# Kernel tuning notes

Measured on AMD Instinct MI355X. Metric: run time of the kernel, lower is better.

## Reference

```python
import jax, jax.numpy as jnp
import numpy as np

B, S, HID, NH = 8, 1024, 1024, 16
HD = HID // NH  # 64
STR = 128
NEG = -1e10


def setup_inputs() -> dict:
    key = jax.random.key(0)
    ks = jax.random.split(key, 16)
    def lin(k, fan_in, fan_out):
        bound = 1.0 / np.sqrt(fan_in)
        kw, kb = jax.random.split(k)
        W = jax.random.uniform(kw, (fan_in, fan_out), jnp.float32, -bound, bound)
        b = jax.random.uniform(kb, (fan_out,), jnp.float32, -bound, bound)
        return W, b
    Wq, bq = lin(ks[0], HID, HID)
    Wk, bk = lin(ks[1], HID, HID)
    Wv, bv = lin(ks[2], HID, HID)
    Wsk, bsk = lin(ks[3], HID, STR)
    Wsv, bsv = lin(ks[4], HID, STR)
    Wo, bo = lin(ks[5], HID + STR, HID)
    return {
        "query": jax.random.normal(ks[6], (B, S, HID), jnp.float32),
        "key": jax.random.normal(ks[7], (B, S, HID), jnp.float32),
        "value": jax.random.normal(ks[8], (B, S, HID), jnp.float32),
        "x_rsa": jax.random.normal(ks[9], (B, S, STR), jnp.float32),
        "mask": jax.random.randint(ks[10], (B, 1, 1, S), 0, 2, jnp.int32),
        "rsa_mask": jax.random.randint(ks[11], (B, 1, 1, S), 0, 2, jnp.int32),
        "Wq": Wq, "bq": bq, "Wk": Wk, "bk": bk, "Wv": Wv, "bv": bv,
        "Wsk": Wsk, "bsk": bsk, "Wsv": Wsv, "bsv": bsv, "Wo": Wo, "bo": bo,
    }


def reference(query, key, value, x_rsa, mask, rsa_mask,
              Wq, bq, Wk, bk, Wv, bv, Wsk, bsk, Wsv, bsv, Wo, bo):
    scale = jnp.sqrt(jnp.float32(HD))
    Q = (query @ Wq + bq).reshape(B, S, NH, HD).transpose(0, 2, 1, 3)   # [B,NH,S,HD]
    K = (key @ Wk + bk).reshape(B, S, NH, HD).transpose(0, 2, 1, 3)
    V = (value @ Wv + bv).reshape(B, S, NH, HD).transpose(0, 2, 1, 3)
    str_K = (key @ Wsk + bsk)[:, None, :, :]    # [B,1,S,128]
    str_V = (value @ Wsv + bsv)[:, None, :, :]
    rsa_Q = x_rsa[:, None, :, :]                # [B,1,S,128]

    energy = jnp.einsum('bhqd,bhkd->bhqk', Q, K)           # [B,NH,S,S]
    rsa_energy = jnp.einsum('bhqd,bhkd->bhqk', rsa_Q, str_K)  # [B,1,S,S]
    # torch order: mask first, then divide by scale
    energy = jnp.where(mask == 0, NEG, energy) / scale
    rsa_energy = jnp.where(mask == 0, NEG, rsa_energy)
    rsa_energy = jnp.where(rsa_mask == 0, NEG, rsa_energy)  # str_scale == 1

    attention = jax.nn.softmax(energy, axis=-1)
    rsa_attention = jax.nn.softmax(rsa_energy, axis=-1)
    # dropout is identity in eval mode
    x = jnp.einsum('bhqk,bhkd->bhqd', attention, V)          # [B,NH,S,HD]
    rsa_x = jnp.einsum('bhqk,bhkd->bhqd', rsa_attention, str_V)  # [B,1,S,128]
    x = x.transpose(0, 2, 1, 3).reshape(B, S, HID)
    rsa_x = rsa_x.transpose(0, 2, 1, 3).reshape(B, S, STR)
    out = jnp.concatenate((x, rsa_x), axis=-1) @ Wo + bo     # [B,S,HID]
    return out, attention, rsa_attention
```

## Files before the change

### kernel.cpp

```cpp
#include <hip/hip_runtime.h>
#include <stdint.h>

typedef unsigned int u32;
typedef _Float16 f16_t;

typedef _Float16 f16x8 __attribute__((ext_vector_type(8)));
typedef float    f32x4 __attribute__((ext_vector_type(4)));

__device__ __forceinline__ f32x4 mfma16(f16x8 a, f16x8 b, f32x4 c){
  return __builtin_amdgcn_mfma_f32_16x16x32_f16(a, b, c, 0, 0, 0);
}
__device__ __forceinline__ float fexp2(float x){ return __builtin_amdgcn_exp2f(x); }

__device__ __forceinline__ void gl_lds16(const void* g, void* l){
  typedef const __attribute__((address_space(1))) void* gasp;
  typedef __attribute__((address_space(3))) void* lasp;
  gasp gp = reinterpret_cast<gasp>(reinterpret_cast<uintptr_t>(g));
  lasp lp = reinterpret_cast<lasp>(static_cast<u32>(reinterpret_cast<uintptr_t>(l)));
  __builtin_amdgcn_global_load_lds(gp, lp, 16, 0, 0);
}

template<int NBYTES, int ROWB, int NT>
__device__ __forceinline__ void stage_swz(const char* gbase, u32 gstrideB, char* lds, int tid){
  const u32 lane = (u32)(tid & 63);
  #pragma unroll
  for (int j = 0; j < NBYTES/(NT*16); ++j){
    u32 o   = (u32)(j*NT + tid) * 16u;
    u32 row = o / (u32)ROWB;
    u32 col = (o % (u32)ROWB) ^ ((row & 7u) << 4);
    gl_lds16(gbase + (size_t)row * gstrideB + col, lds + (o - lane*16u));
  }
}

__device__ __forceinline__ f16x8 frag_ld(const char* lds, u32 row, u32 rowB, u32 kbyte){
  return *reinterpret_cast<const f16x8*>(lds + (size_t)row*rowB + (kbyte ^ ((row & 7u) << 4)));
}

__device__ __forceinline__ void cvt8(const float* __restrict__ in, f16_t* __restrict__ out, u32 i){
  const f32x4* p = reinterpret_cast<const f32x4*>(in) + 2*(size_t)i;
  f32x4 a = p[0], b = p[1];
  f16x8 v;
  v[0]=(f16_t)a[0]; v[1]=(f16_t)a[1]; v[2]=(f16_t)a[2]; v[3]=(f16_t)a[3];
  v[4]=(f16_t)b[0]; v[5]=(f16_t)b[1]; v[6]=(f16_t)b[2]; v[7]=(f16_t)b[3];
  *(reinterpret_cast<f16x8*>(out) + i) = v;
}

__global__ void prep_all(const float* __restrict__ q, const float* __restrict__ k,
                         const float* __restrict__ v, const float* __restrict__ xr,
                         const int* __restrict__ mask, const int* __restrict__ rmask,
                         f16_t* __restrict__ qo, f16_t* __restrict__ ko,
                         f16_t* __restrict__ vo, f16_t* __restrict__ xo,
                         float* __restrict__ mb, float* __restrict__ rb){
  u32 b = blockIdx.x;
  if (b < 12288u){
    const float* in; f16_t* out; u32 base;
    if (b < 4096u){ in=q; out=qo; base=0u; }
    else if (b < 8192u){ in=k; out=ko; base=4096u; }
    else { in=v; out=vo; base=8192u; }
    cvt8(in, out, (b-base)*256u + threadIdx.x);
  } else if (b < 12800u){
    cvt8(xr, xo, (b-12288u)*256u + threadIdx.x);
  } else {
    u32 i = (b-12800u)*256u + threadIdx.x;
    int m = mask[i]; int r = rmask[i];
    mb[i] = m ? 0.0f : -1.0e9f;
    rb[i] = (m && r) ? 0.0f : -1.0e9f;
  }
}

__global__ void transpose_cvt(const float* __restrict__ W0, const float* __restrict__ W1,
                              const float* __restrict__ W2,
                              f16_t* __restrict__ T0, f16_t* __restrict__ T1, f16_t* __restrict__ T2,
                              u32 K, u32 N){
  const float* W = blockIdx.z==0 ? W0 : blockIdx.z==1 ? W1 : W2;
  f16_t* WT      = blockIdx.z==0 ? T0 : blockIdx.z==1 ? T1 : T2;
  __shared__ float tile[32][33];
  const u32 k0 = blockIdx.x*32u, n0 = blockIdx.y*32u;
  const int t = threadIdx.x;
  const int r = t >> 3, c4 = (t & 7) * 4;
  f32x4 v = *reinterpret_cast<const f32x4*>(W + (size_t)(k0 + r)*N + n0 + c4);
  tile[r][c4+0]=v[0]; tile[r][c4+1]=v[1]; tile[r][c4+2]=v[2]; tile[r][c4+3]=v[3];
  __syncthreads();
  union { f16_t x[4]; uint64_t u; } pk;
  #pragma unroll
  for (int j=0;j<4;++j) pk.x[j] = (f16_t)tile[c4+j][r];
  *reinterpret_cast<uint64_t*>(WT + (size_t)(n0 + r)*K + k0 + c4) = pk.u;
}

struct GArg { const void* A; const void* Bt; const float* bias; void* C; u32 ldc; int mode; };

__global__ __launch_bounds__(256, 2)
void gemm_bt(GArg g0, GArg g1, GArg g2, u32 lda, u32 ldb, u32 K)
{
  __shared__ char As[2][16384];
  __shared__ char Bs[2][16384];
  GArg g = blockIdx.z==0 ? g0 : blockIdx.z==1 ? g1 : g2;
  const int tid = threadIdx.x, lane = tid & 63, wid = tid >> 6;
  const int wr = wid >> 1, wc = wid & 1;
  const u32 bn = blockIdx.x * 128u, bm = blockIdx.y * 128u;
  const char* Ab = (const char*)((const f16_t*)g.A + (size_t)bm * lda);
  const char* Bb = (const char*)((const f16_t*)g.Bt + (size_t)bn * ldb);
  const u32 ldaB = lda*2u, ldbB = ldb*2u;

  f32x4 acc[4][4] = {};
  const int nt = (int)(K >> 6);

  stage_swz<16384,128,256>(Ab, ldaB, As[0], tid);
  stage_swz<16384,128,256>(Bb, ldbB, Bs[0], tid);
  __syncthreads();

  for (int t = 0; t < nt; ++t){
    if (t + 1 < nt){
      stage_swz<16384,128,256>(Ab + (size_t)(t+1)*128, ldaB, As[(t+1)&1], tid);
      stage_swz<16384,128,256>(Bb + (size_t)(t+1)*128, ldbB, Bs[(t+1)&1], tid);
    }
    const char* as = As[t&1]; const char* bs = Bs[t&1];
    f16x8 af[4][2], bf[4][2];
    #pragma unroll
    for (int mi=0; mi<4; ++mi)
      #pragma unroll
      for (int ks=0; ks<2; ++ks)
        af[mi][ks] = frag_ld(as, (u32)(wr*64 + mi*16 + (lane&15)), 128u, (u32)(ks*64 + ((lane>>4)<<4)));
    #pragma unroll
    for (int ni=0; ni<4; ++ni)
      #pragma unroll
      for (int ks=0; ks<2; ++ks)
        bf[ni][ks] = frag_ld(bs, (u32)(wc*64 + ni*16 + (lane&15)), 128u, (u32)(ks*64 + ((lane>>4)<<4)));
    #pragma unroll
    for (int mi=0; mi<4; ++mi)
      #pragma unroll
      for (int ni=0; ni<4; ++ni)
        #pragma unroll
        for (int ks=0; ks<2; ++ks)
          acc[mi][ni] = mfma16(af[mi][ks], bf[ni][ks], acc[mi][ni]);
    __syncthreads();
  }

  float bv[4];
  #pragma unroll
  for (int ni=0; ni<4; ++ni) bv[ni] = g.bias[bn + wc*64 + ni*16 + (lane&15)];

  #pragma unroll
  for (int mi=0; mi<4; ++mi){
    #pragma unroll
    for (int ni=0; ni<4; ++ni){
      u32 n  = bn + (u32)(wc*64 + ni*16 + (lane&15));
      u32 m0 = bm + (u32)(wr*64 + mi*16 + ((lane>>4)<<2));
      if (g.mode == 0){
        float* C = (float*)g.C;
        #pragma unroll
        for (int r=0;r<4;++r) C[(size_t)(m0+r)*g.ldc + n] = acc[mi][ni][r] + bv[ni];
      } else if (g.mode == 1){
        f16_t* C = (f16_t*)g.C;
        #pragma unroll
        for (int r=0;r<4;++r){
          u32 m = m0 + r;
          size_t idx = (((size_t)(m>>10)*16 + (n>>6))*1024 + (m&1023))*64 + (n&63);
          C[idx] = (f16_t)(acc[mi][ni][r] + bv[ni]);
        }
      } else if (g.mode == 2){
        f16_t* C = (f16_t*)g.C;
        size_t idx0 = ((size_t)(m0>>10)*g.ldc + n)*1024 + (m0 & 1023);
        union { f16_t v[4]; uint64_t u; } pk;
        #pragma unroll
        for (int r=0;r<4;++r) pk.v[r] = (f16_t)(acc[mi][ni][r] + bv[ni]);
        *reinterpret_cast<uint64_t*>(C + idx0) = pk.u;
      } else {
        f16_t* C = (f16_t*)g.C;
        #pragma unroll
        for (int r=0;r<4;++r) C[(size_t)(m0+r)*g.ldc + n] = (f16_t)(acc[mi][ni][r] + bv[ni]);
      }
    }
  }
}

template<int D, int BSHIFT, int SCALEBIT>
__global__ __launch_bounds__(512)
void attn_pass1(const f16_t* __restrict__ Qg, const f16_t* __restrict__ Kg,
                const float* __restrict__ mbias, float* __restrict__ statR)
{
  constexpr int S = 1024, KCH = 64;
  constexpr u32 ROWB = D*2;
  __shared__ char Qs[128*D*2];
  __shared__ char Ks[2][KCH*D*2];
  __shared__ float wsum[2][128];

  const int tid = threadIdx.x, lane = tid & 63, wid = tid >> 6;
  const int wr = wid >> 2, wc = wid & 3;
  const u32 qt = blockIdx.x, batch = blockIdx.y;
  const float scale = SCALEBIT ? 0.1803368801111244f : 1.4426950408889634f;
  const f16_t* qb = Qg + ((size_t)batch*S + (size_t)qt*128)*D;
  const f16_t* kb = Kg + (size_t)batch*S*D;
  const float* mbb = mbias + (size_t)(batch >> BSHIFT)*S;

  stage_swz<128*D*2, (int)ROWB, 512>((const char*)qb, ROWB, Qs, tid);
  stage_swz<KCH*D*2, (int)ROWB, 512>((const char*)kb, ROWB, Ks[0], tid);
  __syncthreads();

  float sacc[2] = {0.0f, 0.0f};
  constexpr int NCH = S / KCH;
  for (int ch = 0; ch < NCH; ++ch){
    if (ch + 1 < NCH)
      stage_swz<KCH*D*2, (int)ROWB, 512>((const char*)(kb + (size_t)(ch+1)*KCH*D), ROWB, Ks[(ch+1)&1], tid);
    const char* ks = Ks[ch&1];

    f32x4 mb[2];
    #pragma unroll
    for (int mi=0; mi<2; ++mi)
      mb[mi] = *reinterpret_cast<const f32x4*>(mbb + ch*KCH + wr*32 + mi*16 + ((lane>>4)<<2));

    f32x4 acc[2][2] = {};
    #pragma unroll
    for (int ksl=0; ksl<D/32; ++ksl){
      f16x8 af[2], bf[2];
      #pragma unroll
      for (int mi=0; mi<2; ++mi)
        af[mi] = frag_ld(ks, (u32)(wr*32 + mi*16 + (lane&15)), ROWB, (u32)(ksl*64 + ((lane>>4)<<4)));
      #pragma unroll
      for (int ni=0; ni<2; ++ni)
        bf[ni] = frag_ld(Qs, (u32)(wc*32 + ni*16 + (lane&15)), ROWB, (u32)(ksl*64 + ((lane>>4)<<4)));
      #pragma unroll
      for (int mi=0; mi<2; ++mi)
        #pragma unroll
        for (int ni=0; ni<2; ++ni)
          acc[mi][ni] = mfma16(af[mi], bf[ni], acc[mi][ni]);
    }

    #pragma unroll
    for (int ni=0; ni<2; ++ni)
      #pragma unroll
      for (int mi=0; mi<2; ++mi)
        #pragma unroll
        for (int r=0;r<4;++r)
          sacc[ni] += fexp2(acc[mi][ni][r]*scale + mb[mi][r]);

    __syncthreads();
  }

  #pragma unroll
  for (int ni=0; ni<2; ++ni){
    float s = sacc[ni];
    s += __shfl_xor(s, 16);
    s += __shfl_xor(s, 32);
    sacc[ni] = s;
  }
  if (lane < 16){
    wsum[wr][wc*32 + lane]      = sacc[0];
    wsum[wr][wc*32 + 16 + lane] = sacc[1];
  }
  __syncthreads();
  if (tid < 128)
    statR[(size_t)batch*S + (size_t)qt*128 + tid] = 1.0f / (wsum[0][tid] + wsum[1][tid]);
}

template<int D, int BSHIFT, int SCALEBIT>
__global__ __launch_bounds__(512)
void attn_pass2(const f16_t* __restrict__ Qg, const f16_t* __restrict__ Kg, const f16_t* __restrict__ Vtg,
                const float* __restrict__ mbias, const float* __restrict__ statR,
                float* __restrict__ attnOut,
                f16_t* __restrict__ xout, u32 xld, u32 xcolAdd)
{
  constexpr int S = 1024, KCH = 64;
  constexpr u32 ROWB = D*2;
  constexpr int MIPV = D/32;
  __shared__ char Qs[128*D*2];
  __shared__ char Ks[2][KCH*D*2];
  __shared__ char Vs[2][D*KCH*2];
  __shared__ float Pout[128*KCH];

  const int tid = threadIdx.x, lane = tid & 63, wid = tid >> 6;
  const int wr = wid >> 2, wc = wid & 3;
  const u32 qt = blockIdx.x, batch = blockIdx.y;
  const u32 bb = batch >> BSHIFT;
  const float scale = SCALEBIT ? 0.1803368801111244f : 1.4426950408889634f;
  const f16_t* qb = Qg + ((size_t)batch*S + (size_t)qt*128)*D;
  const f16_t* kb = Kg + (size_t)batch*S*D;
  const char* vtb = (const char*)(Vtg + (size_t)batch*D*S);
  const float* mbb = mbias + (size_t)bb*S;
  char* poutb = (char*)Pout;

  float rreg[2];
  #pragma unroll
  for (int ni=0; ni<2; ++ni){
    u32 q = qt*128u + (u32)(wc*32 + ni*16 + (lane&15));
    rreg[ni] = statR[(size_t)batch*S + q];
  }
  f32x4 accX[MIPV][2] = {};

  stage_swz<128*D*2, (int)ROWB, 512>((const char*)qb, ROWB, Qs, tid);
  stage_swz<KCH*D*2, (int)ROWB, 512>((const char*)kb, ROWB, Ks[0], tid);
  stage_swz<D*KCH*2, 128, 512>(vtb, (u32)(S*2), Vs[0], tid);
  __syncthreads();

  constexpr int NCH = S / KCH;
  for (int ch = 0; ch < NCH; ++ch){
    if (ch + 1 < NCH){
      stage_swz<KCH*D*2, (int)ROWB, 512>((const char*)(kb + (size_t)(ch+1)*KCH*D), ROWB, Ks[(ch+1)&1], tid);
      stage_swz<D*KCH*2, 128, 512>(vtb + (size_t)(ch+1)*KCH*2, (u32)(S*2), Vs[(ch+1)&1], tid);
    }
    const char* ks = Ks[ch&1];
    const char* vs = Vs[ch&1];

    f32x4 mb[2];
    #pragma unroll
    for (int mi=0; mi<2; ++mi)
      mb[mi] = *reinterpret_cast<const f32x4*>(mbb + ch*KCH + wr*32 + mi*16 + ((lane>>4)<<2));

    f32x4 acc[2][2] = {};
    #pragma unroll
    for (int ksl=0; ksl<D/32; ++ksl){
      f16x8 af[2], bf[2];
      #pragma unroll
      for (int mi=0; mi<2; ++mi)
        af[mi] = frag_ld(ks, (u32)(wr*32 + mi*16 + (lane&15)), ROWB, (u32)(ksl*64 + ((lane>>4)<<4)));
      #pragma unroll
      for (int ni=0; ni<2; ++ni)
        bf[ni] = frag_ld(Qs, (u32)(wc*32 + ni*16 + (lane&15)), ROWB, (u32)(ksl*64 + ((lane>>4)<<4)));
      #pragma unroll
      for (int mi=0; mi<2; ++mi)
        #pragma unroll
        for (int ni=0; ni<2; ++ni)
          acc[mi][ni] = mfma16(af[mi], bf[ni], acc[mi][ni]);
    }

    #pragma unroll
    for (int ni=0; ni<2; ++ni){
      u32 q = (u32)(wc*32 + ni*16 + (lane&15));
      #pragma unroll
      for (int mi=0; mi<2; ++mi){
        f32x4 pv;
        #pragma unroll
        for (int r=0;r<4;++r)
          pv[r] = fexp2(acc[mi][ni][r]*scale + mb[mi][r]) * rreg[ni];
        u32 k0b = (u32)(wr*32 + mi*16 + ((lane>>4)<<2)) * 4u;
        *reinterpret_cast<f32x4*>(poutb + (size_t)q*256 + (k0b ^ ((q&7u)<<4))) = pv;
      }
    }
    __syncthreads();

    #pragma unroll
    for (int ksl=0; ksl<2; ++ksl){
      f16x8 pb[2];
      #pragma unroll
      for (int ni=0; ni<2; ++ni){
        u32 q = (u32)(wc*32 + ni*16 + (lane&15));
        u32 kb0 = (u32)(ksl*128 + ((lane>>4)<<5));
        f32x4 p0 = *reinterpret_cast<const f32x4*>(poutb + (size_t)q*256 + ((kb0      ) ^ ((q&7u)<<4)));
        f32x4 p1 = *reinterpret_cast<const f32x4*>(poutb + (size_t)q*256 + ((kb0 + 16u) ^ ((q&7u)<<4)));
        f16x8 v;
        v[0]=(f16_t)p0[0]; v[1]=(f16_t)p0[1]; v[2]=(f16_t)p0[2]; v[3]=(f16_t)p0[3];
        v[4]=(f16_t)p1[0]; v[5]=(f16_t)p1[1]; v[6]=(f16_t)p1[2]; v[7]=(f16_t)p1[3];
        pb[ni] = v;
      }
      #pragma unroll
      for (int mi=0; mi<MIPV; ++mi){
        f16x8 vf = frag_ld(vs, (u32)(wr*(D/2) + mi*16 + (lane&15)), 128u, (u32)(ksl*64 + ((lane>>4)<<4)));
        #pragma unroll
        for (int ni=0; ni<2; ++ni)
          accX[mi][ni] = mfma16(vf, pb[ni], accX[mi][ni]);
      }
    }

    {
      u32 q2 = (u32)tid >> 2;
      float* abase = attnOut + (size_t)batch*S*S + ((size_t)qt*128 + q2)*S + (size_t)ch*KCH;
      #pragma unroll
      for (int j=0;j<4;++j){
        u32 kbyte = ((u32)(tid&3) + 4u*(u32)j)*16u;
        f32x4 v = *reinterpret_cast<const f32x4*>(poutb + (size_t)q2*256 + (kbyte ^ ((q2&7u)<<4)));
        *reinterpret_cast<f32x4*>(abase + (kbyte>>2)) = v;
      }
    }
    __syncthreads();
  }

  u32 col0 = (batch & ((1u<<BSHIFT)-1u)) * (u32)D + xcolAdd;
  #pragma unroll
  for (int mi=0; mi<MIPV; ++mi){
    #pragma unroll
    for (int ni=0; ni<2; ++ni){
      u32 d = (u32)(wr*(D/2) + mi*16 + ((lane>>4)<<2));
      u32 q = qt*128u + (u32)(wc*32 + ni*16 + (lane&15));
      union { f16_t v[4]; uint64_t u; } pk;
      #pragma unroll
      for (int r=0;r<4;++r) pk.v[r] = (f16_t)accX[mi][ni][r];
      *reinterpret_cast<uint64_t*>(xout + ((size_t)bb*S + q)*xld + col0 + d) = pk.u;
    }
  }
}

extern "C" void kernel_launch(void* const* d_in, const int* in_sizes, int n_in,
                              void* d_out, int out_size, void* d_ws, size_t ws_size,
                              hipStream_t stream)
{
  const float* query = (const float*)d_in[0];
  const float* key   = (const float*)d_in[1];
  const float* value = (const float*)d_in[2];
  const float* x_rsa = (const float*)d_in[3];
  const int*   mask  = (const int*)d_in[4];
  const int*   rmask = (const int*)d_in[5];
  const float* Wq = (const float*)d_in[6];  const float* bq = (const float*)d_in[7];
  const float* Wk = (const float*)d_in[8];  const float* bk = (const float*)d_in[9];
  const float* Wv = (const float*)d_in[10]; const float* bv = (const float*)d_in[11];
  const float* Wsk= (const float*)d_in[12]; const float* bsk= (const float*)d_in[13];
  const float* Wsv= (const float*)d_in[14]; const float* bsv= (const float*)d_in[15];
  const float* Wo = (const float*)d_in[16]; const float* bo = (const float*)d_in[17];

  char* ws = (char*)d_ws;
  size_t off = 0;
  auto alloc = [&](size_t bytes)->char*{ char* p = ws + off; off += (bytes + 255) & ~(size_t)255; return p; };

  f16_t* q16  = (f16_t*)alloc(16777216);
  f16_t* k16  = (f16_t*)alloc(16777216);
  f16_t* v16  = (f16_t*)alloc(16777216);
  f16_t* xrf  = (f16_t*)alloc(2097152);
  f16_t* wqT  = (f16_t*)alloc(2097152);
  f16_t* wkT  = (f16_t*)alloc(2097152);
  f16_t* wvT  = (f16_t*)alloc(2097152);
  f16_t* wskT = (f16_t*)alloc(262144);
  f16_t* wsvT = (f16_t*)alloc(262144);
  f16_t* woT  = (f16_t*)alloc(2359296);
  f16_t* Qh   = (f16_t*)alloc(16777216);
  f16_t* Kh   = (f16_t*)alloc(16777216);
  f16_t* Vth  = (f16_t*)alloc(16777216);
  f16_t* strK = (f16_t*)alloc(2097152);
  f16_t* strVt= (f16_t*)alloc(2097152);
  f16_t* conc = (f16_t*)alloc(18874368);
  float* stRm = (float*)alloc(524288);
  float* stRr = (float*)alloc(32768);
  float* mbias= (float*)alloc(32768);
  float* rbias= (float*)alloc(32768);

  prep_all<<<12832,256,0,stream>>>(query, key, value, x_rsa, mask, rmask,
                                   q16, k16, v16, xrf, mbias, rbias);
  transpose_cvt<<<dim3(32,32,3),256,0,stream>>>(Wq, Wk, Wv, wqT, wkT, wvT, 1024, 1024);
  transpose_cvt<<<dim3(32,4,2), 256,0,stream>>>(Wsk, Wsv, Wsv, wskT, wsvT, wsvT, 1024, 128);
  transpose_cvt<<<dim3(36,32,1),256,0,stream>>>(Wo, Wo, Wo, woT, woT, woT, 1152, 1024);

  {
    GArg gq{q16, wqT, bq, Qh,  0,    1};
    GArg gk{k16, wkT, bk, Kh,  0,    1};
    GArg gv{v16, wvT, bv, Vth, 1024, 2};
    gemm_bt<<<dim3(8,64,3),256,0,stream>>>(gq, gk, gv, 1024, 1024, 1024);
  }
  {
    GArg gk{k16, wskT, bsk, strK,  128, 3};
    GArg gv{v16, wsvT, bsv, strVt, 128, 2};
    gemm_bt<<<dim3(1,64,2),256,0,stream>>>(gk, gv, gv, 1024, 1024, 1024);
  }

  attn_pass1<64,4,1> <<<dim3(8,128),512,0,stream>>>(Qh,  Kh,   mbias, stRm);
  attn_pass1<128,0,0><<<dim3(8,8),  512,0,stream>>>(xrf, strK, rbias, stRr);

  float* outp  = (float*)d_out;
  float* attnp = outp + 8388608;
  float* rsap  = outp + 8388608 + 134217728;

  attn_pass2<64,4,1> <<<dim3(8,128),512,0,stream>>>(Qh,  Kh,   Vth,   mbias, stRm, attnp, conc, 1152, 0);
  attn_pass2<128,0,0><<<dim3(8,8),  512,0,stream>>>(xrf, strK, strVt, rbias, stRr, rsap,  conc, 1152, 1024);

  {
    GArg go{conc, woT, bo, outp, 1024, 0};
    gemm_bt<<<dim3(8,64,1),256,0,stream>>>(go, go, go, 1152, 1152, 1152);
  }

  (void)in_sizes; (void)n_in; (void)out_size; (void)ws_size;
}
```

Measured before the change: 428.7 us.

## Merge launches: fuse weight transposes, GEMMs and attention passes into fewer kernels

Weight transpose-conversion moves into the prep kernel. All five projection GEMMs run in one grid. The main and RSA attention passes each become a single launch, which cuts kernel count and the tail idle time between small launches. The RSA path now uses a 32-key chunk so both attention variants fit in a shared LDS size. The GEMM swaps MFMA operands for the non-transposed outputs so the epilogue can write vectorized rows, and the swizzle is generalized to the row width. This adds branchy dispatch and larger static LDS for the attention kernels, which may lower occupancy for the main heads.

```diff
diff --git a/kernel.cpp b/kernel.cpp
--- a/kernel.cpp
+++ b/kernel.cpp
@@ -27,13 +27,19 @@
   for (int j = 0; j < NBYTES/(NT*16); ++j){
     u32 o   = (u32)(j*NT + tid) * 16u;
     u32 row = o / (u32)ROWB;
-    u32 col = (o % (u32)ROWB) ^ ((row & 7u) << 4);
+    u32 col = (o % (u32)ROWB) ^ ((row & ((u32)(ROWB>>4)-1u)) << 4);
     gl_lds16(gbase + (size_t)row * gstrideB + col, lds + (o - lane*16u));
   }
 }
 
-__device__ __forceinline__ f16x8 frag_ld(const char* lds, u32 row, u32 rowB, u32 kbyte){
-  return *reinterpret_cast<const f16x8*>(lds + (size_t)row*rowB + (kbyte ^ ((row & 7u) << 4)));
+template<int ROWB>
+__device__ __forceinline__ u32 swzb(u32 row, u32 col){
+  return col ^ ((row & ((u32)(ROWB>>4)-1u)) << 4);
+}
+
+template<int ROWB>
+__device__ __forceinline__ f16x8 frag_ld(const char* lds, u32 row, u32 kbyte){
+  return *reinterpret_cast<const f16x8*>(lds + (size_t)row*ROWB + swzb<ROWB>(row, kbyte));
 }
 
 __device__ __forceinline__ void cvt8(const float* __restrict__ in, f16_t* __restrict__ out, u32 i){
@@ -50,7 +56,14 @@
                          const int* __restrict__ mask, const int* __restrict__ rmask,
                          f16_t* __restrict__ qo, f16_t* __restrict__ ko,
                          f16_t* __restrict__ vo, f16_t* __restrict__ xo,
-                         float* __restrict__ mb, float* __restrict__ rb){
+                         float* __restrict__ mb, float* __restrict__ rb,
+                         const float* __restrict__ Wq, const float* __restrict__ Wk,
+                         const float* __restrict__ Wv, const float* __restrict__ Wsk,
+                         const float* __restrict__ Wsv, const float* __restrict__ Wo,
+                         f16_t* __restrict__ wqT, f16_t* __restrict__ wkT, f16_t* __restrict__ wvT,
+                         f16_t* __restrict__ wskT, f16_t* __restrict__ wsvT, f16_t* __restrict__ woT)
+{
+  __shared__ float tile[32][33];
   u32 b = blockIdx.x;
   if (b < 12288u){
     const float* in; f16_t* out; u32 base;
@@ -60,50 +73,65 @@
     cvt8(in, out, (b-base)*256u + threadIdx.x);
   } else if (b < 12800u){
     cvt8(xr, xo, (b-12288u)*256u + threadIdx.x);
-  } else {
+  } else if (b < 12832u){
     u32 i = (b-12800u)*256u + threadIdx.x;
     int m = mask[i]; int r = rmask[i];
     mb[i] = m ? 0.0f : -1.0e9f;
     rb[i] = (m && r) ? 0.0f : -1.0e9f;
-  }
-}
-
-__global__ void transpose_cvt(const float* __restrict__ W0, const float* __restrict__ W1,
-                              const float* __restrict__ W2,
-                              f16_t* __restrict__ T0, f16_t* __restrict__ T1, f16_t* __restrict__ T2,
-                              u32 K, u32 N){
-  const float* W = blockIdx.z==0 ? W0 : blockIdx.z==1 ? W1 : W2;
-  f16_t* WT      = blockIdx.z==0 ? T0 : blockIdx.z==1 ? T1 : T2;
-  __shared__ float tile[32][33];
-  const u32 k0 = blockIdx.x*32u, n0 = blockIdx.y*32u;
-  const int t = threadIdx.x;
-  const int r = t >> 3, c4 = (t & 7) * 4;
-  f32x4 v = *reinterpret_cast<const f32x4*>(W + (size_t)(k0 + r)*N + n0 + c4);
-  tile[r][c4+0]=v[0]; tile[r][c4+1]=v[1]; tile[r][c4+2]=v[2]; tile[r][c4+3]=v[3];
-  __syncthreads();
-  union { f16_t x[4]; uint64_t u; } pk;
-  #pragma unroll
-  for (int j=0;j<4;++j) pk.x[j] = (f16_t)tile[c4+j][r];
-  *reinterpret_cast<uint64_t*>(WT + (size_t)(n0 + r)*K + k0 + c4) = pk.u;
-}
-
-struct GArg { const void* A; const void* Bt; const float* bias; void* C; u32 ldc; int mode; };
+  } else {
+    u32 t = b - 12832u;
+    const float* W; f16_t* WT; u32 K, N, i, j;
+    if (t < 3072u){
+      u32 w = t >> 10, l = t & 1023u;
+      W = w==0 ? Wq : w==1 ? Wk : Wv;
+      WT = w==0 ? wqT : w==1 ? wkT : wvT;
+      K = 1024u; N = 1024u; i = l & 31u; j = l >> 5;
+    } else if (t < 3328u){
+      u32 l = t - 3072u;
+      W  = l < 128u ? Wsk : Wsv;
+      WT = l < 128u ? wskT : wsvT;
+      l &= 127u;
+      K = 1024u; N = 128u; i = l & 31u; j = l >> 5;
+    } else {
+      u32 l = t - 3328u;
+      W = Wo; WT = woT; K = 1152u; N = 1024u; i = l % 36u; j = l / 36u;
+    }
+    const u32 k0 = i*32u, n0 = j*32u;
+    const int tt = threadIdx.x;
+    const int r = tt >> 3, c4 = (tt & 7) * 4;
+    f32x4 val = *reinterpret_cast<const f32x4*>(W + (size_t)(k0 + r)*N + n0 + c4);
+    tile[r][c4+0]=val[0]; tile[r][c4+1]=val[1]; tile[r][c4+2]=val[2]; tile[r][c4+3]=val[3];
+    __syncthreads();
+    union { f16_t x[4]; uint64_t u; } pk;
+    #pragma unroll
+    for (int jj=0;jj<4;++jj) pk.x[jj] = (f16_t)tile[c4+jj][r];
+    *reinterpret_cast<uint64_t*>(WT + (size_t)(n0 + r)*K + k0 + c4) = pk.u;
+  }
+}
+
+struct GArg { const f16_t* A; const f16_t* Bt; const float* bias; void* C; u32 lda, ldb, ldc, K; int mode; };
+struct GPack { GArg g[5]; int single; };
 
 __global__ __launch_bounds__(256, 2)
-void gemm_bt(GArg g0, GArg g1, GArg g2, u32 lda, u32 ldb, u32 K)
+void gemm_bt(GPack p)
 {
   __shared__ char As[2][16384];
   __shared__ char Bs[2][16384];
-  GArg g = blockIdx.z==0 ? g0 : blockIdx.z==1 ? g1 : g2;
+  GArg g; u32 bn;
+  const u32 bm = blockIdx.y * 128u;
+  if (p.single >= 0){ g = p.g[p.single]; bn = blockIdx.x*128u; }
+  else if (blockIdx.z == 0u){ if (blockIdx.x >= 2u) return; g = p.g[3u+blockIdx.x]; bn = 0u; }
+  else { g = p.g[blockIdx.z-1u]; bn = blockIdx.x*128u; }
+
   const int tid = threadIdx.x, lane = tid & 63, wid = tid >> 6;
   const int wr = wid >> 1, wc = wid & 1;
-  const u32 bn = blockIdx.x * 128u, bm = blockIdx.y * 128u;
-  const char* Ab = (const char*)((const f16_t*)g.A + (size_t)bm * lda);
-  const char* Bb = (const char*)((const f16_t*)g.Bt + (size_t)bn * ldb);
-  const u32 ldaB = lda*2u, ldbB = ldb*2u;
+  const char* Ab = (const char*)(g.A + (size_t)bm * g.lda);
+  const char* Bb = (const char*)(g.Bt + (size_t)bn * g.ldb);
+  const u32 ldaB = g.lda*2u, ldbB = g.ldb*2u;
+  const bool swp = (g.mode != 2);
 
   f32x4 acc[4][4] = {};
-  const int nt = (int)(K >> 6);
+  const int nt = (int)(g.K >> 6);
 
   stage_swz<16384,128,256>(Ab, ldaB, As[0], tid);
   stage_swz<16384,128,256>(Bb, ldbB, Bs[0], tid);
@@ -120,107 +148,133 @@
     for (int mi=0; mi<4; ++mi)
       #pragma unroll
       for (int ks=0; ks<2; ++ks)
-        af[mi][ks] = frag_ld(as, (u32)(wr*64 + mi*16 + (lane&15)), 128u, (u32)(ks*64 + ((lane>>4)<<4)));
+        af[mi][ks] = frag_ld<128>(as, (u32)(wr*64 + mi*16 + (lane&15)), (u32)(ks*64 + ((lane>>4)<<4)));
     #pragma unroll
     for (int ni=0; ni<4; ++ni)
       #pragma unroll
       for (int ks=0; ks<2; ++ks)
-        bf[ni][ks] = frag_ld(bs, (u32)(wc*64 + ni*16 + (lane&15)), 128u, (u32)(ks*64 + ((lane>>4)<<4)));
-    #pragma unroll
-    for (int mi=0; mi<4; ++mi)
-      #pragma unroll
-      for (int ni=0; ni<4; ++ni)
-        #pragma unroll
-        for (int ks=0; ks<2; ++ks)
-          acc[mi][ni] = mfma16(af[mi][ks], bf[ni][ks], acc[mi][ni]);
+        bf[ni][ks] = frag_ld<128>(bs, (u32)(wc*64 + ni*16 + (lane&15)), (u32)(ks*64 + ((lane>>4)<<4)));
+    if (swp){
+      #pragma unroll
+      for (int mi=0; mi<4; ++mi)
+        #pragma unroll
+        for (int ni=0; ni<4; ++ni)
+          #pragma unroll
+          for (int ks=0; ks<2; ++ks)
+            acc[mi][ni] = mfma16(bf[ni][ks], af[mi][ks], acc[mi][ni]);
+    } else {
+      #pragma unroll
+      for (int mi=0; mi<4; ++mi)
+        #pragma unroll
+        for (int ni=0; ni<4; ++ni)
+          #pragma unroll
+          for (int ks=0; ks<2; ++ks)
+            acc[mi][ni] = mfma16(af[mi][ks], bf[ni][ks], acc[mi][ni]);
+    }
     __syncthreads();
   }
 
-  float bv[4];
-  #pragma unroll
-  for (int ni=0; ni<4; ++ni) bv[ni] = g.bias[bn + wc*64 + ni*16 + (lane&15)];
-
-  #pragma unroll
-  for (int mi=0; mi<4; ++mi){
-    #pragma unroll
-    for (int ni=0; ni<4; ++ni){
-      u32 n  = bn + (u32)(wc*64 + ni*16 + (lane&15));
-      u32 m0 = bm + (u32)(wr*64 + mi*16 + ((lane>>4)<<2));
-      if (g.mode == 0){
-        float* C = (float*)g.C;
-        #pragma unroll
-        for (int r=0;r<4;++r) C[(size_t)(m0+r)*g.ldc + n] = acc[mi][ni][r] + bv[ni];
-      } else if (g.mode == 1){
-        f16_t* C = (f16_t*)g.C;
-        #pragma unroll
-        for (int r=0;r<4;++r){
-          u32 m = m0 + r;
-          size_t idx = (((size_t)(m>>10)*16 + (n>>6))*1024 + (m&1023))*64 + (n&63);
-          C[idx] = (f16_t)(acc[mi][ni][r] + bv[ni]);
-        }
-      } else if (g.mode == 2){
-        f16_t* C = (f16_t*)g.C;
+  if (g.mode == 2){
+    float bv[4];
+    #pragma unroll
+    for (int ni=0; ni<4; ++ni) bv[ni] = g.bias[bn + wc*64 + ni*16 + (lane&15)];
+    f16_t* C = (f16_t*)g.C;
+    #pragma unroll
+    for (int mi=0; mi<4; ++mi){
+      #pragma unroll
+      for (int ni=0; ni<4; ++ni){
+        u32 n  = bn + (u32)(wc*64 + ni*16 + (lane&15));
+        u32 m0 = bm + (u32)(wr*64 + mi*16 + ((lane>>4)<<2));
         size_t idx0 = ((size_t)(m0>>10)*g.ldc + n)*1024 + (m0 & 1023);
         union { f16_t v[4]; uint64_t u; } pk;
         #pragma unroll
         for (int r=0;r<4;++r) pk.v[r] = (f16_t)(acc[mi][ni][r] + bv[ni]);
         *reinterpret_cast<uint64_t*>(C + idx0) = pk.u;
-      } else {
-        f16_t* C = (f16_t*)g.C;
-        #pragma unroll
-        for (int r=0;r<4;++r) C[(size_t)(m0+r)*g.ldc + n] = (f16_t)(acc[mi][ni][r] + bv[ni]);
       }
     }
-  }
-}
-
-template<int D, int BSHIFT, int SCALEBIT>
-__global__ __launch_bounds__(512)
-void attn_pass1(const f16_t* __restrict__ Qg, const f16_t* __restrict__ Kg,
-                const float* __restrict__ mbias, float* __restrict__ statR)
-{
-  constexpr int S = 1024, KCH = 64;
-  constexpr u32 ROWB = D*2;
-  __shared__ char Qs[128*D*2];
-  __shared__ char Ks[2][KCH*D*2];
-  __shared__ float wsum[2][128];
-
-  const int tid = threadIdx.x, lane = tid & 63, wid = tid >> 6;
+  } else {
+    f32x4 bf4[4];
+    #pragma unroll
+    for (int ni=0; ni<4; ++ni)
+      bf4[ni] = *reinterpret_cast<const f32x4*>(g.bias + bn + wc*64 + ni*16 + ((lane>>4)<<2));
+    #pragma unroll
+    for (int mi=0; mi<4; ++mi){
+      u32 m = bm + (u32)(wr*64 + mi*16 + (lane&15));
+      #pragma unroll
+      for (int ni=0; ni<4; ++ni){
+        u32 n0 = bn + (u32)(wc*64 + ni*16 + ((lane>>4)<<2));
+        if (g.mode == 0){
+          float* C = (float*)g.C;
+          f32x4 v = acc[mi][ni] + bf4[ni];
+          *reinterpret_cast<f32x4*>(C + (size_t)m*g.ldc + n0) = v;
+        } else if (g.mode == 1){
+          f16_t* C = (f16_t*)g.C;
+          size_t idx = (((size_t)(m>>10)*16 + (n0>>6))*1024 + (m&1023))*64 + (n0&63);
+          union { f16_t v[4]; uint64_t u; } pk;
+          #pragma unroll
+          for (int r=0;r<4;++r) pk.v[r] = (f16_t)(acc[mi][ni][r] + bf4[ni][r]);
+          *reinterpret_cast<uint64_t*>(C + idx) = pk.u;
+        } else {
+          f16_t* C = (f16_t*)g.C;
+          union { f16_t v[4]; uint64_t u; } pk;
+          #pragma unroll
+          for (int r=0;r<4;++r) pk.v[r] = (f16_t)(acc[mi][ni][r] + bf4[ni][r]);
+          *reinterpret_cast<uint64_t*>(C + (size_t)m*g.ldc + n0) = pk.u;
+        }
+      }
+    }
+  }
+}
+
+template<int D, int KCH, int BSHIFT, int SCALEBIT>
+__device__ __forceinline__ void pass1_body(char* smem,
+    const f16_t* __restrict__ Qg, const f16_t* __restrict__ Kg,
+    const float* __restrict__ mbias, float* __restrict__ statR,
+    const int tid, const u32 qt, const u32 batch)
+{
+  constexpr int S = 1024;
+  constexpr int ROWB = D*2;
+  constexpr int MI = KCH/32;
+  char* Qs  = smem;
+  char* Ks0 = smem + 128*ROWB;
+  char* Ks1 = Ks0 + KCH*ROWB;
+  float* wsum = (float*)(Ks1 + KCH*ROWB);
+
+  const int lane = tid & 63, wid = tid >> 6;
   const int wr = wid >> 2, wc = wid & 3;
-  const u32 qt = blockIdx.x, batch = blockIdx.y;
   const float scale = SCALEBIT ? 0.1803368801111244f : 1.4426950408889634f;
   const f16_t* qb = Qg + ((size_t)batch*S + (size_t)qt*128)*D;
   const f16_t* kb = Kg + (size_t)batch*S*D;
   const float* mbb = mbias + (size_t)(batch >> BSHIFT)*S;
 
-  stage_swz<128*D*2, (int)ROWB, 512>((const char*)qb, ROWB, Qs, tid);
-  stage_swz<KCH*D*2, (int)ROWB, 512>((const char*)kb, ROWB, Ks[0], tid);
+  stage_swz<128*ROWB, ROWB, 512>((const char*)qb, ROWB, Qs, tid);
+  stage_swz<KCH*ROWB, ROWB, 512>((const char*)kb, ROWB, Ks0, tid);
   __syncthreads();
 
   float sacc[2] = {0.0f, 0.0f};
   constexpr int NCH = S / KCH;
   for (int ch = 0; ch < NCH; ++ch){
     if (ch + 1 < NCH)
-      stage_swz<KCH*D*2, (int)ROWB, 512>((const char*)(kb + (size_t)(ch+1)*KCH*D), ROWB, Ks[(ch+1)&1], tid);
-    const char* ks = Ks[ch&1];
-
-    f32x4 mb[2];
-    #pragma unroll
-    for (int mi=0; mi<2; ++mi)
-      mb[mi] = *reinterpret_cast<const f32x4*>(mbb + ch*KCH + wr*32 + mi*16 + ((lane>>4)<<2));
-
-    f32x4 acc[2][2] = {};
+      stage_swz<KCH*ROWB, ROWB, 512>((const char*)(kb + (size_t)(ch+1)*KCH*D), ROWB, ((ch+1)&1)?Ks1:Ks0, tid);
+    const char* ks = (ch&1) ? Ks1 : Ks0;
+
+    f32x4 mb[MI];
+    #pragma unroll
+    for (int mi=0; mi<MI; ++mi)
+      mb[mi] = *reinterpret_cast<const f32x4*>(mbb + ch*KCH + wr*(KCH/2) + mi*16 + ((lane>>4)<<2));
+
+    f32x4 acc[MI][2] = {};
     #pragma unroll
     for (int ksl=0; ksl<D/32; ++ksl){
-      f16x8 af[2], bf[2];
-      #pragma unroll
-      for (int mi=0; mi<2; ++mi)
-        af[mi] = frag_ld(ks, (u32)(wr*32 + mi*16 + (lane&15)), ROWB, (u32)(ksl*64 + ((lane>>4)<<4)));
+      f16x8 af[MI], bf[2];
+      #pragma unroll
+      for (int mi=0; mi<MI; ++mi)
+        af[mi] = frag_ld<ROWB>(ks, (u32)(wr*(KCH/2) + mi*16 + (lane&15)), (u32)(ksl*64 + ((lane>>4)<<4)));
       #pragma unroll
       for (int ni=0; ni<2; ++ni)
-        bf[ni] = frag_ld(Qs, (u32)(wc*32 + ni*16 + (lane&15)), ROWB, (u32)(ksl*64 + ((lane>>4)<<4)));
-      #pragma unroll
-      for (int mi=0; mi<2; ++mi)
+        bf[ni] = frag_ld<ROWB>(Qs, (u32)(wc*32 + ni*16 + (lane&15)), (u32)(ksl*64 + ((lane>>4)<<4)));
+      #pragma unroll
+      for (int mi=0; mi<MI; ++mi)
         #pragma unroll
         for (int ni=0; ni<2; ++ni)
           acc[mi][ni] = mfma16(af[mi], bf[ni], acc[mi][ni]);
@@ -229,7 +283,7 @@
     #pragma unroll
     for (int ni=0; ni<2; ++ni)
       #pragma unroll
-      for (int mi=0; mi<2; ++mi)
+      for (int mi=0; mi<MI; ++mi)
         #pragma unroll
         for (int r=0;r<4;++r)
           sacc[ni] += fexp2(acc[mi][ni][r]*scale + mb[mi][r]);
@@ -245,39 +299,42 @@
     sacc[ni] = s;
   }
   if (lane < 16){
-    wsum[wr][wc*32 + lane]      = sacc[0];
-    wsum[wr][wc*32 + 16 + lane] = sacc[1];
+    wsum[wr*128 + wc*32 + lane]      = sacc[0];
+    wsum[wr*128 + wc*32 + 16 + lane] = sacc[1];
   }
   __syncthreads();
   if (tid < 128)
-    statR[(size_t)batch*S + (size_t)qt*128 + tid] = 1.0f / (wsum[0][tid] + wsum[1][tid]);
-}
-
-template<int D, int BSHIFT, int SCALEBIT>
-__global__ __launch_bounds__(512)
-void attn_pass2(const f16_t* __restrict__ Qg, const f16_t* __restrict__ Kg, const f16_t* __restrict__ Vtg,
-                const float* __restrict__ mbias, const float* __restrict__ statR,
-                float* __restrict__ attnOut,
-                f16_t* __restrict__ xout, u32 xld, u32 xcolAdd)
-{
-  constexpr int S = 1024, KCH = 64;
-  constexpr u32 ROWB = D*2;
+    statR[(size_t)batch*S + (size_t)qt*128 + tid] = 1.0f / (wsum[tid] + wsum[128 + tid]);
+}
+
+template<int D, int KCH, int BSHIFT, int SCALEBIT>
+__device__ __forceinline__ void pass2_body(char* smem,
+    const f16_t* __restrict__ Qg, const f16_t* __restrict__ Kg, const f16_t* __restrict__ Vtg,
+    const float* __restrict__ mbias, const float* __restrict__ statR,
+    float* __restrict__ attnOut, f16_t* __restrict__ xout, u32 xld, u32 xcolAdd,
+    const int tid, const u32 qt, const u32 batch)
+{
+  constexpr int S = 1024;
+  constexpr int ROWB = D*2;
+  constexpr int ROWBV = KCH*2;
+  constexpr int PROW = KCH*4;
+  constexpr int MI = KCH/32;
   constexpr int MIPV = D/32;
-  __shared__ char Qs[128*D*2];
-  __shared__ char Ks[2][KCH*D*2];
-  __shared__ char Vs[2][D*KCH*2];
-  __shared__ float Pout[128*KCH];
-
-  const int tid = threadIdx.x, lane = tid & 63, wid = tid >> 6;
+  char* Qs  = smem;
+  char* Ks0 = Qs + 128*ROWB;
+  char* Ks1 = Ks0 + KCH*ROWB;
+  char* Vs0 = Ks1 + KCH*ROWB;
+  char* Vs1 = Vs0 + D*KCH*2;
+  char* poutb = Vs1 + D*KCH*2;
+
+  const int lane = tid & 63, wid = tid >> 6;
   const int wr = wid >> 2, wc = wid & 3;
-  const u32 qt = blockIdx.x, batch = blockIdx.y;
   const u32 bb = batch >> BSHIFT;
   const float scale = SCALEBIT ? 0.1803368801111244f : 1.4426950408889634f;
   const f16_t* qb = Qg + ((size_t)batch*S + (size_t)qt*128)*D;
   const f16_t* kb = Kg + (size_t)batch*S*D;
   const char* vtb = (const char*)(Vtg + (size_t)batch*D*S);
   const float* mbb = mbias + (size_t)bb*S;
-  char* poutb = (char*)Pout;
 
   float rreg[2];
   #pragma unroll
@@ -287,37 +344,37 @@
   }
   f32x4 accX[MIPV][2] = {};
 
-  stage_swz<128*D*2, (int)ROWB, 512>((const char*)qb, ROWB, Qs, tid);
-  stage_swz<KCH*D*2, (int)ROWB, 512>((const char*)kb, ROWB, Ks[0], tid);
-  stage_swz<D*KCH*2, 128, 512>(vtb, (u32)(S*2), Vs[0], tid);
+  stage_swz<128*ROWB, ROWB, 512>((const char*)qb, ROWB, Qs, tid);
+  stage_swz<KCH*ROWB, ROWB, 512>((const char*)kb, ROWB, Ks0, tid);
+  stage_swz<D*KCH*2, ROWBV, 512>(vtb, (u32)(S*2), Vs0, tid);
   __syncthreads();
 
   constexpr int NCH = S / KCH;
   for (int ch = 0; ch < NCH; ++ch){
     if (ch + 1 < NCH){
-      stage_swz<KCH*D*2, (int)ROWB, 512>((const char*)(kb + (size_t)(ch+1)*KCH*D), ROWB, Ks[(ch+1)&1], tid);
-      stage_swz<D*KCH*2, 128, 512>(vtb + (size_t)(ch+1)*KCH*2, (u32)(S*2), Vs[(ch+1)&1], tid);
-    }
-    const char* ks = Ks[ch&1];
-    const char* vs = Vs[ch&1];
-
-    f32x4 mb[2];
-    #pragma unroll
-    for (int mi=0; mi<2; ++mi)
-      mb[mi] = *reinterpret_cast<const f32x4*>(mbb + ch*KCH + wr*32 + mi*16 + ((lane>>4)<<2));
-
-    f32x4 acc[2][2] = {};
+      stage_swz<KCH*ROWB, ROWB, 512>((const char*)(kb + (size_t)(ch+1)*KCH*D), ROWB, ((ch+1)&1)?Ks1:Ks0, tid);
+      stage_swz<D*KCH*2, ROWBV, 512>(vtb + (size_t)(ch+1)*KCH*2, (u32)(S*2), ((ch+1)&1)?Vs1:Vs0, tid);
+    }
+    const char* ks = (ch&1) ? Ks1 : Ks0;
+    const char* vs = (ch&1) ? Vs1 : Vs0;
+
+    f32x4 mb[MI];
+    #pragma unroll
+    for (int mi=0; mi<MI; ++mi)
+      mb[mi] = *reinterpret_cast<const f32x4*>(mbb + ch*KCH + wr*(KCH/2) + mi*16 + ((lane>>4)<<2));
+
+    f32x4 acc[MI][2] = {};
     #pragma unroll
     for (int ksl=0; ksl<D/32; ++ksl){
-      f16x8 af[2], bf[2];
-      #pragma unroll
-      for (int mi=0; mi<2; ++mi)
-        af[mi] = frag_ld(ks, (u32)(wr*32 + mi*16 + (lane&15)), ROWB, (u32)(ksl*64 + ((lane>>4)<<4)));
+      f16x8 af[MI], bf[2];
+      #pragma unroll
+      for (int mi=0; mi<MI; ++mi)
+        af[mi] = frag_ld<ROWB>(ks, (u32)(wr*(KCH/2) + mi*16 + (lane&15)), (u32)(ksl*64 + ((lane>>4)<<4)));
       #pragma unroll
       for (int ni=0; ni<2; ++ni)
-        bf[ni] = frag_ld(Qs, (u32)(wc*32 + ni*16 + (lane&15)), ROWB, (u32)(ksl*64 + ((lane>>4)<<4)));
-      #pragma unroll
-      for (int mi=0; mi<2; ++mi)
+        bf[ni] = frag_ld<ROWB>(Qs, (u32)(wc*32 + ni*16 + (lane&15)), (u32)(ksl*64 + ((lane>>4)<<4)));
+      #pragma unroll
+      for (int mi=0; mi<MI; ++mi)
         #pragma unroll
         for (int ni=0; ni<2; ++ni)
           acc[mi][ni] = mfma16(af[mi], bf[ni], acc[mi][ni]);
@@ -327,26 +384,26 @@
     for (int ni=0; ni<2; ++ni){
       u32 q = (u32)(wc*32 + ni*16 + (lane&15));
       #pragma unroll
-      for (int mi=0; mi<2; ++mi){
+      for (int mi=0; mi<MI; ++mi){
         f32x4 pv;
         #pragma unroll
         for (int r=0;r<4;++r)
           pv[r] = fexp2(acc[mi][ni][r]*scale + mb[mi][r]) * rreg[ni];
-        u32 k0b = (u32)(wr*32 + mi*16 + ((lane>>4)<<2)) * 4u;
-        *reinterpret_cast<f32x4*>(poutb + (size_t)q*256 + (k0b ^ ((q&7u)<<4))) = pv;
+        u32 k0b = (u32)(wr*(KCH/2) + mi*16 + ((lane>>4)<<2)) * 4u;
+        *reinterpret_cast<f32x4*>(poutb + (size_t)q*PROW + swzb<PROW>(q, k0b)) = pv;
       }
     }
     __syncthreads();
 
     #pragma unroll
-    for (int ksl=0; ksl<2; ++ksl){
+    for (int ksl=0; ksl<KCH/32; ++ksl){
       f16x8 pb[2];
       #pragma unroll
       for (int ni=0; ni<2; ++ni){
         u32 q = (u32)(wc*32 + ni*16 + (lane&15));
         u32 kb0 = (u32)(ksl*128 + ((lane>>4)<<5));
-        f32x4 p0 = *reinterpret_cast<const f32x4*>(poutb + (size_t)q*256 + ((kb0      ) ^ ((q&7u)<<4)));
-        f32x4 p1 = *reinterpret_cast<const f32x4*>(poutb + (size_t)q*256 + ((kb0 + 16u) ^ ((q&7u)<<4)));
+        f32x4 p0 = *reinterpret_cast<const f32x4*>(poutb + (size_t)q*PROW + swzb<PROW>(q, kb0));
+        f32x4 p1 = *reinterpret_cast<const f32x4*>(poutb + (size_t)q*PROW + swzb<PROW>(q, kb0 + 16u));
         f16x8 v;
         v[0]=(f16_t)p0[0]; v[1]=(f16_t)p0[1]; v[2]=(f16_t)p0[2]; v[3]=(f16_t)p0[3];
         v[4]=(f16_t)p1[0]; v[5]=(f16_t)p1[1]; v[6]=(f16_t)p1[2]; v[7]=(f16_t)p1[3];
@@ -354,7 +411,7 @@
       }
       #pragma unroll
       for (int mi=0; mi<MIPV; ++mi){
-        f16x8 vf = frag_ld(vs, (u32)(wr*(D/2) + mi*16 + (lane&15)), 128u, (u32)(ksl*64 + ((lane>>4)<<4)));
+        f16x8 vf = frag_ld<ROWBV>(vs, (u32)(wr*(D/2) + mi*16 + (lane&15)), (u32)(ksl*64 + ((lane>>4)<<4)));
         #pragma unroll
         for (int ni=0; ni<2; ++ni)
           accX[mi][ni] = mfma16(vf, pb[ni], accX[mi][ni]);
@@ -365,9 +422,9 @@
       u32 q2 = (u32)tid >> 2;
       float* abase = attnOut + (size_t)batch*S*S + ((size_t)qt*128 + q2)*S + (size_t)ch*KCH;
       #pragma unroll
-      for (int j=0;j<4;++j){
+      for (int j=0; j<KCH/16; ++j){
         u32 kbyte = ((u32)(tid&3) + 4u*(u32)j)*16u;
-        f32x4 v = *reinterpret_cast<const f32x4*>(poutb + (size_t)q2*256 + (kbyte ^ ((q2&7u)<<4)));
+        f32x4 v = *reinterpret_cast<const f32x4*>(poutb + (size_t)q2*PROW + swzb<PROW>(q2, kbyte));
         *reinterpret_cast<f32x4*>(abase + (kbyte>>2)) = v;
       }
     }
@@ -387,6 +444,35 @@
       *reinterpret_cast<uint64_t*>(xout + ((size_t)bb*S + q)*xld + col0 + d) = pk.u;
     }
   }
+}
+
+__global__ __launch_bounds__(512)
+void attn_pass1_all(const f16_t* __restrict__ Qh, const f16_t* __restrict__ Kh,
+                    const float* __restrict__ mbias, float* __restrict__ stRm,
+                    const f16_t* __restrict__ xrf, const f16_t* __restrict__ strK,
+                    const float* __restrict__ rbias, float* __restrict__ stRr)
+{
+  __shared__ char smem[50176];
+  const int tid = threadIdx.x;
+  const u32 qt = blockIdx.x, y = blockIdx.y;
+  if (y < 8u) pass1_body<128,32,0,0>(smem, xrf, strK, rbias, stRr, tid, qt, y);
+  else        pass1_body<64, 64,4,1>(smem, Qh,  Kh,   mbias, stRm, tid, qt, y-8u);
+}
+
+__global__ __launch_bounds__(512)
+void attn_pass2_all(const f16_t* __restrict__ Qh, const f16_t* __restrict__ Kh,
+                    const f16_t* __restrict__ Vth, const float* __restrict__ mbias,
+                    const float* __restrict__ stRm, float* __restrict__ attnp,
+                    const f16_t* __restrict__ xrf, const f16_t* __restrict__ strK,
+                    const f16_t* __restrict__ strVt, const float* __restrict__ rbias,
+                    const float* __restrict__ stRr, float* __restrict__ rsap,
+                    f16_t* __restrict__ conc)
+{
+  __shared__ char smem[81920];
+  const int tid = threadIdx.x;
+  const u32 qt = blockIdx.x, y = blockIdx.y;
+  if (y < 8u) pass2_body<128,32,0,0>(smem, xrf, strK, strVt, rbias, stRr, rsap, conc, 1152u, 1024u, tid, qt, y);
+  else        pass2_body<64, 64,4,1>(smem, Qh,  Kh,   Vth,   mbias, stRm, attnp, conc, 1152u, 0u,    tid, qt, y-8u);
 }
 
 extern "C" void kernel_launch(void* const* d_in, const int* in_sizes, int n_in,
@@ -431,37 +517,37 @@
   float* mbias= (float*)alloc(32768);
   float* rbias= (float*)alloc(32768);
 
-  prep_all<<<12832,256,0,stream>>>(query, key, value, x_rsa, mask, rmask,
-                                   q16, k16, v16, xrf, mbias, rbias);
-  transpose_cvt<<<dim3(32,32,3),256,0,stream>>>(Wq, Wk, Wv, wqT, wkT, wvT, 1024, 1024);
-  transpose_cvt<<<dim3(32,4,2), 256,0,stream>>>(Wsk, Wsv, Wsv, wskT, wsvT, wsvT, 1024, 128);
-  transpose_cvt<<<dim3(36,32,1),256,0,stream>>>(Wo, Wo, Wo, woT, woT, woT, 1152, 1024);
+  prep_all<<<17312,256,0,stream>>>(query, key, value, x_rsa, mask, rmask,
+                                   q16, k16, v16, xrf, mbias, rbias,
+                                   Wq, Wk, Wv, Wsk, Wsv, Wo,
+                                   wqT, wkT, wvT, wskT, wsvT, woT);
 
   {
-    GArg gq{q16, wqT, bq, Qh,  0,    1};
-    GArg gk{k16, wkT, bk, Kh,  0,    1};
-    GArg gv{v16, wvT, bv, Vth, 1024, 2};
-    gemm_bt<<<dim3(8,64,3),256,0,stream>>>(gq, gk, gv, 1024, 1024, 1024);
-  }
-  {
-    GArg gk{k16, wskT, bsk, strK,  128, 3};
-    GArg gv{v16, wsvT, bsv, strVt, 128, 2};
-    gemm_bt<<<dim3(1,64,2),256,0,stream>>>(gk, gv, gv, 1024, 1024, 1024);
-  }
-
-  attn_pass1<64,4,1> <<<dim3(8,128),512,0,stream>>>(Qh,  Kh,   mbias, stRm);
-  attn_pass1<128,0,0><<<dim3(8,8),  512,0,stream>>>(xrf, strK, rbias, stRr);
+    GPack pm{};
+    pm.g[0] = {q16, wqT,  bq,  (void*)Qh,    1024u,1024u,0u,   1024u, 1};
+    pm.g[1] = {k16, wkT,  bk,  (void*)Kh,    1024u,1024u,0u,   1024u, 1};
+    pm.g[2] = {v16, wvT,  bv,  (void*)Vth,   1024u,1024u,1024u,1024u, 2};
+    pm.g[3] = {k16, wskT, bsk, (void*)strK,  1024u,1024u,128u, 1024u, 3};
+    pm.g[4] = {v16, wsvT, bsv, (void*)strVt, 1024u,1024u,128u, 1024u, 2};
+    pm.single = -1;
+    gemm_bt<<<dim3(8,64,4),256,0,stream>>>(pm);
+  }
 
   float* outp  = (float*)d_out;
   float* attnp = outp + 8388608;
   float* rsap  = outp + 8388608 + 134217728;
 
-  attn_pass2<64,4,1> <<<dim3(8,128),512,0,stream>>>(Qh,  Kh,   Vth,   mbias, stRm, attnp, conc, 1152, 0);
-  attn_pass2<128,0,0><<<dim3(8,8),  512,0,stream>>>(xrf, strK, strVt, rbias, stRr, rsap,  conc, 1152, 1024);
+  attn_pass1_all<<<dim3(8,136),512,0,stream>>>(Qh, Kh, mbias, stRm, xrf, strK, rbias, stRr);
+
+  attn_pass2_all<<<dim3(8,136),512,0,stream>>>(Qh, Kh, Vth, mbias, stRm, attnp,
+                                               xrf, strK, strVt, rbias, stRr, rsap, conc);
 
   {
-    GArg go{conc, woT, bo, outp, 1024, 0};
-    gemm_bt<<<dim3(8,64,1),256,0,stream>>>(go, go, go, 1152, 1152, 1152);
+    GPack po{};
+    po.g[0] = {conc, woT, bo, (void*)outp, 1152u,1152u,1024u,1152u, 0};
+    po.g[1] = po.g[0]; po.g[2] = po.g[0]; po.g[3] = po.g[0]; po.g[4] = po.g[0];
+    po.single = 0;
+    gemm_bt<<<dim3(8,64,1),256,0,stream>>>(po);
   }
 
   (void)in_sizes; (void)n_in; (void)out_size; (void)ws_size;
```

After: 397.7 us. 1.08x faster.
